# Kernel optimization log

Measured on AMD Instinct MI355X. Metric: run time of the kernel, lower is better.

Reference implementation:

```python
import jax, jax.numpy as jnp
import numpy as np

B, T, D, H, MLP_DIM = 4, 1024, 768, 12, 3072


def setup_inputs() -> dict:
    key = jax.random.key(0)
    ks = jax.random.split(key, 16)
    s = 0.02
    def n(i, shape):
        return jax.random.normal(ks[i], shape, jnp.float32) * s
    inp = {
        "x": jax.random.normal(ks[0], (B, T, D), jnp.float32),
        "y": jax.random.normal(ks[1], (B, T, D), jnp.float32),
        # self-attention (stream a = x, stream b = y), bias-free Linears
        "w_qkv_a": n(2, (D, 3 * D)), "w_out_a": n(3, (D, D)),
        "w_qkv_b": n(4, (D, 3 * D)), "w_out_b": n(5, (D, D)),
        # cross-attention
        "cw_qkv_a": n(6, (D, 3 * D)), "cw_out_a": n(7, (D, D)),
        "cw_qkv_b": n(8, (D, 3 * D)), "cw_out_b": n(9, (D, D)),
        # MLPs (Linear with bias)
        "mlp_a_w1": n(10, (D, MLP_DIM)), "mlp_a_b1": jnp.zeros((MLP_DIM,), jnp.float32),
        "mlp_a_w2": n(11, (MLP_DIM, D)), "mlp_a_b2": jnp.zeros((D,), jnp.float32),
        "mlp_b_w1": n(12, (D, MLP_DIM)), "mlp_b_b1": jnp.zeros((MLP_DIM,), jnp.float32),
        "mlp_b_w2": n(13, (MLP_DIM, D)), "mlp_b_b2": jnp.zeros((D,), jnp.float32),
    }
    for i in range(1, 7):
        inp[f"ln{i}_g"] = jnp.ones((D,), jnp.float32)
        inp[f"ln{i}_b"] = jnp.zeros((D,), jnp.float32)
    return inp


def _ln(x, g, b, eps=1e-5):
    m = x.mean(-1, keepdims=True)
    v = x.var(-1, keepdims=True)
    return (x - m) / jnp.sqrt(v + eps) * g + b


def _split_qkv(x, w, h):
    # faithful to einops 'b t (d k h) -> k b h t d' (d outermost, h innermost)
    qkv = x @ w                      # [b, t, 3D]
    b, t, _ = qkv.shape
    d = w.shape[0] // h
    qkv = qkv.reshape(b, t, d, 3, h).transpose(3, 0, 4, 1, 2)  # [3, b, h, t, d]
    return qkv[0], qkv[1], qkv[2]


def _attend(q, k, v, dk):
    a = jax.nn.softmax(jnp.einsum('bhid,bhjd->bhij', q, k) / dk, axis=-1)
    o = jnp.einsum('bhij,bhjd->bhid', a, v)
    b, h, t, d = o.shape
    return o.transpose(0, 2, 1, 3).reshape(b, t, h * d)


def reference(x, y,
              w_qkv_a, w_out_a, w_qkv_b, w_out_b,
              cw_qkv_a, cw_out_a, cw_qkv_b, cw_out_b,
              mlp_a_w1, mlp_a_b1, mlp_a_w2, mlp_a_b2,
              mlp_b_w1, mlp_b_b1, mlp_b_w2, mlp_b_b2,
              ln1_g, ln1_b, ln2_g, ln2_b, ln3_g, ln3_b,
              ln4_g, ln4_b, ln5_g, ln5_b, ln6_g, ln6_b):
    dk = np.float32(np.sqrt(D / H))
    # --- self-attention stage (pre-LN, residual); dropout = identity (eval) ---
    _x = _ln(x, ln1_g, ln1_b)
    _y = _ln(y, ln4_g, ln4_b)
    q, k, v = _split_qkv(_x, w_qkv_a, H)
    x = x + _attend(q, k, v, dk) @ w_out_a
    q, k, v = _split_qkv(_y, w_qkv_b, H)
    y = y + _attend(q, k, v, dk) @ w_out_b
    # --- cross-attention stage ---
    _x = _ln(x, ln2_g, ln2_b)
    _y = _ln(y, ln5_g, ln5_b)
    q1, k1, v1 = _split_qkv(_x, cw_qkv_a, H)
    q2, k2, v2 = _split_qkv(_y, cw_qkv_b, H)
    x = x + _attend(q2, k1, v1, dk) @ cw_out_a   # query from y, k/v from x
    y = y + _attend(q1, k2, v2, dk) @ cw_out_b   # query from x, k/v from y
    # --- MLP stage ---
    _x = _ln(x, ln3_g, ln3_b)
    _y = _ln(y, ln6_g, ln6_b)
    x = x + (jax.nn.gelu(_x @ mlp_a_w1 + mlp_a_b1, approximate=False) @ mlp_a_w2 + mlp_a_b2)
    y = y + (jax.nn.gelu(_y @ mlp_b_w1 + mlp_b_b1, approximate=False) @ mlp_b_w2 + mlp_b_b2)
    return (x, y)
```

## Files before the change

### kernel.cpp

```cpp
#include <hip/hip_runtime.h>
#include <hip/hip_bf16.h>

using bf16 = __hip_bfloat16;
typedef __bf16 bf16x8 __attribute__((ext_vector_type(8)));
typedef float f32x4 __attribute__((ext_vector_type(4)));

#define DEV __device__ __forceinline__

DEV void gload16(const void* g, void* l) {
  __builtin_amdgcn_global_load_lds((__attribute__((address_space(1))) void*)(g),
                                   (__attribute__((address_space(3))) void*)(l), 16, 0, 0);
}

DEV void mfma16(int4 a, int4 b, f32x4& c) {
  c = __builtin_amdgcn_mfma_f32_16x16x32_bf16(
      __builtin_bit_cast(bf16x8, a), __builtin_bit_cast(bf16x8, b), c, 0, 0, 0);
}

DEV unsigned short bfb(float x) { return __builtin_bit_cast(unsigned short, __float2bfloat16(x)); }

template<bool PERM>
__global__ __launch_bounds__(256) void wconv(const float* __restrict__ s0, const float* __restrict__ s1,
                                             const float* __restrict__ s2, const float* __restrict__ s3,
                                             bf16* d0, bf16* d1, bf16* d2, bf16* d3, int K, int N) {
  const float* S[4] = {s0, s1, s2, s3};
  bf16* Dd[4] = {d0, d1, d2, d3};
  const float* __restrict__ src = S[blockIdx.z];
  bf16* __restrict__ dst = Dd[blockIdx.z];
  __shared__ float tile[32][33];
  int tx = threadIdx.x, ty = threadIdx.y;
  int n0 = blockIdx.x * 32, k0 = blockIdx.y * 32;
#pragma unroll
  for (int i = 0; i < 4; i++) tile[ty + 8 * i][tx] = src[(size_t)(k0 + ty + 8 * i) * N + n0 + tx];
  __syncthreads();
#pragma unroll
  for (int i = 0; i < 4; i++) {
    int n = n0 + ty + 8 * i;
    int np;
    if (PERM) {
      int dd = n / 36; int r = n - dd * 36; int kk = r / 12; int h = r - kk * 12;
      np = kk * 768 + h * 64 + dd;
    } else np = n;
    dst[(size_t)np * K + k0 + tx] = __float2bfloat16(tile[tx][ty + 8 * i]);
  }
}

__global__ __launch_bounds__(192) void ln2(const float* __restrict__ xa, const float* __restrict__ xb,
                                           const float* __restrict__ ga, const float* __restrict__ ba,
                                           const float* __restrict__ gb, const float* __restrict__ bb,
                                           bf16* __restrict__ out) {
  int row = blockIdx.x;
  int s = row >> 12, r = row & 4095;
  const float* __restrict__ src = s ? xb : xa;
  const float* __restrict__ gp = s ? gb : ga;
  const float* __restrict__ bp = s ? bb : ba;
  int tid = threadIdx.x;
  float4 v = ((const float4*)(src + (size_t)r * 768))[tid];
  float sum = v.x + v.y + v.z + v.w;
  float sq = v.x * v.x + v.y * v.y + v.z * v.z + v.w * v.w;
#pragma unroll
  for (int o = 32; o; o >>= 1) { sum += __shfl_down(sum, o); sq += __shfl_down(sq, o); }
  __shared__ float red[6];
  int wv = tid >> 6;
  if ((tid & 63) == 0) { red[wv] = sum; red[wv + 3] = sq; }
  __syncthreads();
  sum = red[0] + red[1] + red[2];
  sq = red[3] + red[4] + red[5];
  float mean = sum * (1.f / 768.f);
  float var = sq * (1.f / 768.f) - mean * mean;
  float rstd = rsqrtf(var + 1e-5f);
  float4 g4 = ((const float4*)gp)[tid], b4 = ((const float4*)bp)[tid];
  ushort4 u;
  u.x = bfb((v.x - mean) * rstd * g4.x + b4.x);
  u.y = bfb((v.y - mean) * rstd * g4.y + b4.y);
  u.z = bfb((v.z - mean) * rstd * g4.z + b4.z);
  u.w = bfb((v.w - mean) * rstd * g4.w + b4.w);
  *(ushort4*)&out[(size_t)row * 768 + tid * 4] = u;
}

template<int EPI>
__global__ __launch_bounds__(256) void gemm_k(const bf16* __restrict__ A0, const bf16* __restrict__ A1,
                                              const bf16* __restrict__ Bt0, const bf16* __restrict__ Bt1,
                                              void* __restrict__ C0, void* __restrict__ C1,
                                              const float* __restrict__ bias0, const float* __restrict__ bias1,
                                              const float* __restrict__ res0, const float* __restrict__ res1,
                                              int N, int K) {
  int s = blockIdx.z;
  const bf16* __restrict__ A = s ? A1 : A0;
  const bf16* __restrict__ Bt = s ? Bt1 : Bt0;
  const float* __restrict__ bias = s ? bias1 : bias0;
  const float* __restrict__ res = s ? res1 : res0;
  int m0 = blockIdx.x * 128, n0 = blockIdx.y * 128;
  int tid = threadIdx.x, lane = tid & 63, w = tid >> 6;
  int g = lane >> 4, li = lane & 15;
  int wm = w >> 1, wn = w & 1;
  __shared__ __align__(16) bf16 As[2][128 * 32];
  __shared__ __align__(16) bf16 Bs[2][128 * 32];
  f32x4 acc[4][4];
  f32x4 zz = {0.f, 0.f, 0.f, 0.f};
#pragma unroll
  for (int i = 0; i < 4; i++)
#pragma unroll
    for (int j = 0; j < 4; j++) acc[i][j] = zz;

  const bf16* Ab = A + (size_t)m0 * K;
  const bf16* Bb = Bt + (size_t)n0 * K;
  int sw = (g ^ (li & 3)) << 3;

  auto stage = [&](int buf, int k0) {
#pragma unroll
    for (int i = 0; i < 2; i++) {
      int unit = w * 64 + i * 256 + lane;
      int row = unit >> 2, up = unit & 3;
      int col = (up ^ (row & 3)) << 3;
      gload16(Ab + (size_t)row * K + k0 + col, &As[buf][w * 512 + i * 2048]);
      gload16(Bb + (size_t)row * K + k0 + col, &Bs[buf][w * 512 + i * 2048]);
    }
  };

  const int nt = K >> 5;
  stage(0, 0);
  int cur = 0;
  for (int t = 0; t < nt; ++t) {
    __syncthreads();
    if (t + 1 < nt) stage(cur ^ 1, (t + 1) << 5);
    int4 af[4], bfr[4];
#pragma unroll
    for (int mi = 0; mi < 4; mi++) af[mi] = *(const int4*)&As[cur][(wm * 64 + mi * 16 + li) * 32 + sw];
#pragma unroll
    for (int ni = 0; ni < 4; ni++) bfr[ni] = *(const int4*)&Bs[cur][(wn * 64 + ni * 16 + li) * 32 + sw];
#pragma unroll
    for (int mi = 0; mi < 4; mi++)
#pragma unroll
      for (int ni = 0; ni < 4; ni++) mfma16(af[mi], bfr[ni], acc[mi][ni]);
    cur ^= 1;
  }

  int mrow0 = m0 + wm * 64;
  int col0 = n0 + wn * 64;
  if constexpr (EPI == 0) {
    bf16* qkv = (bf16*)C0;
#pragma unroll
    for (int mi = 0; mi < 4; mi++) {
      int mr = mrow0 + mi * 16 + 4 * g;
      int b = mr >> 10, t = mr & 1023;
#pragma unroll
      for (int ni = 0; ni < 4; ni++) {
        int col = col0 + ni * 16 + li;
        int kk = col / 768; int hd = col - kk * 768; int h = hd >> 6; int dd = hd & 63;
        size_t base = ((size_t)(kk * 2 + s) * 48 + b * 12 + h) * 65536;
        f32x4 v = acc[mi][ni];
        if (kk == 2) {
          ushort4 u; u.x = bfb(v[0]); u.y = bfb(v[1]); u.z = bfb(v[2]); u.w = bfb(v[3]);
          *(ushort4*)&qkv[base + (size_t)dd * 1024 + t] = u;
        } else {
#pragma unroll
          for (int ri = 0; ri < 4; ri++)
            qkv[base + (size_t)(t + ri) * 64 + dd] = __float2bfloat16(v[ri]);
        }
      }
    }
  } else if constexpr (EPI == 1) {
    float* C = (float*)(s ? C1 : C0);
#pragma unroll
    for (int mi = 0; mi < 4; mi++) {
      int mr = mrow0 + mi * 16 + 4 * g;
#pragma unroll
      for (int ni = 0; ni < 4; ni++) {
        int col = col0 + ni * 16 + li;
        float bv = bias ? bias[col] : 0.f;
#pragma unroll
        for (int ri = 0; ri < 4; ri++)
          C[(size_t)(mr + ri) * N + col] = res[(size_t)(mr + ri) * N + col] + acc[mi][ni][ri] + bv;
      }
    }
  } else {
    bf16* C = (bf16*)(s ? C1 : C0);
#pragma unroll
    for (int mi = 0; mi < 4; mi++) {
      int mr = mrow0 + mi * 16 + 4 * g;
#pragma unroll
      for (int ni = 0; ni < 4; ni++) {
        int col = col0 + ni * 16 + li;
        float bv = bias[col];
#pragma unroll
        for (int ri = 0; ri < 4; ri++) {
          float h = acc[mi][ni][ri] + bv;
          float o = 0.5f * h * (1.f + erff(h * 0.70710678118f));
          C[(size_t)(mr + ri) * N + col] = __float2bfloat16(o);
        }
      }
    }
  }
}

__global__ __launch_bounds__(256) void attn_k(const bf16* __restrict__ qkv, bf16* __restrict__ out, int cross) {
  int f = blockIdx.x;
  int qt = (f >> 3) & 7;
  int c = ((f >> 6) << 3) | (f & 7);
  int so = (c >= 48) ? 1 : 0;
  int bh = c - so * 48;
  int qs = cross ? 1 - so : so;
  const bf16* __restrict__ qp = qkv + ((size_t)qs * 48 + bh) * 65536;
  const bf16* __restrict__ kp = qkv + ((size_t)(2 + so) * 48 + bh) * 65536;
  const bf16* __restrict__ vp = qkv + ((size_t)(4 + so) * 48 + bh) * 65536;
  int tid = threadIdx.x, lane = tid & 63, w = tid >> 6, g = lane >> 4, li = lane & 15;
  __shared__ __align__(16) bf16 Ps[4][32 * 64];
  bf16* ps = Ps[w];
  int qr0 = qt * 128 + w * 32;
  int4 qf[2][2];
#pragma unroll
  for (int mi = 0; mi < 2; mi++)
#pragma unroll
    for (int ks = 0; ks < 2; ks++)
      qf[mi][ks] = *(const int4*)(qp + (size_t)(qr0 + mi * 16 + li) * 64 + ks * 32 + 8 * g);
  f32x4 o_acc[2][4];
  float m_run[2], l_run[2];
  f32x4 zz = {0.f, 0.f, 0.f, 0.f};
#pragma unroll
  for (int mi = 0; mi < 2; mi++) {
#pragma unroll
    for (int dj = 0; dj < 4; dj++) o_acc[mi][dj] = zz;
    m_run[mi] = -1e30f; l_run[mi] = 0.f;
  }
  const float C2 = 0.18033688011112042f;
  const int xsw = (li & 7);

#pragma unroll 2
  for (int kt = 0; kt < 16; ++kt) {
    f32x4 sacc[4][2];
#pragma unroll
    for (int nj = 0; nj < 4; nj++) { sacc[nj][0] = zz; sacc[nj][1] = zz; }
#pragma unroll
    for (int nj = 0; nj < 4; nj++) {
      const bf16* krow = kp + (size_t)(kt * 64 + nj * 16 + li) * 64 + 8 * g;
      int4 kf0 = *(const int4*)(krow);
      int4 kf1 = *(const int4*)(krow + 32);
      mfma16(kf0, qf[0][0], sacc[nj][0]); mfma16(kf1, qf[0][1], sacc[nj][0]);
      mfma16(kf0, qf[1][0], sacc[nj][1]); mfma16(kf1, qf[1][1], sacc[nj][1]);
    }
#pragma unroll
    for (int mi = 0; mi < 2; mi++) {
      float mx = sacc[0][mi][0];
#pragma unroll
      for (int nj = 0; nj < 4; nj++)
#pragma unroll
        for (int ri = 0; ri < 4; ri++) mx = fmaxf(mx, sacc[nj][mi][ri]);
      mx = fmaxf(mx, __shfl_xor(mx, 16));
      mx = fmaxf(mx, __shfl_xor(mx, 32));
      float mold = m_run[mi];
      float mnew = mold;
      if (!__all(mx <= mold)) {
        mnew = fmaxf(mold, mx);
        float alpha = exp2f((mold - mnew) * C2);
        l_run[mi] *= alpha;
#pragma unroll
        for (int dj = 0; dj < 4; dj++) o_acc[mi][dj] *= alpha;
        m_run[mi] = mnew;
      }
      float rs = 0.f;
#pragma unroll
      for (int nj = 0; nj < 4; nj++) {
        float p0 = exp2f((sacc[nj][mi][0] - mnew) * C2);
        float p1 = exp2f((sacc[nj][mi][1] - mnew) * C2);
        float p2 = exp2f((sacc[nj][mi][2] - mnew) * C2);
        float p3 = exp2f((sacc[nj][mi][3] - mnew) * C2);
        rs += (p0 + p1) + (p2 + p3);
        ushort4 u; u.x = bfb(p0); u.y = bfb(p1); u.z = bfb(p2); u.w = bfb(p3);
        *(ushort4*)&ps[(mi * 16 + li) * 64 + (((2 * nj + (g >> 1)) ^ xsw) << 3) + ((g & 1) << 2)] = u;
      }
      rs += __shfl_xor(rs, 16);
      rs += __shfl_xor(rs, 32);
      l_run[mi] += rs;
    }
#pragma unroll
    for (int ks2 = 0; ks2 < 2; ks2++) {
      int4 pa0 = *(const int4*)&ps[(0 * 16 + li) * 64 + (((4 * ks2 + g) ^ xsw) << 3)];
      int4 pa1 = *(const int4*)&ps[(1 * 16 + li) * 64 + (((4 * ks2 + g) ^ xsw) << 3)];
#pragma unroll
      for (int dj = 0; dj < 4; dj++) {
        int4 vf = *(const int4*)(vp + (size_t)(dj * 16 + li) * 1024 + kt * 64 + ks2 * 32 + 8 * g);
        mfma16(vf, pa0, o_acc[0][dj]);
        mfma16(vf, pa1, o_acc[1][dj]);
      }
    }
  }
  int b = bh / 12, h = bh - (bh / 12) * 12;
#pragma unroll
  for (int mi = 0; mi < 2; mi++) {
    float inv = 1.f / l_run[mi];
    int tq = qr0 + mi * 16 + li;
    size_t rowbase = ((size_t)so * 4096 + (size_t)b * 1024 + tq) * 768;
#pragma unroll
    for (int dj = 0; dj < 4; dj++) {
      ushort4 u;
      u.x = bfb(o_acc[mi][dj][0] * inv); u.y = bfb(o_acc[mi][dj][1] * inv);
      u.z = bfb(o_acc[mi][dj][2] * inv); u.w = bfb(o_acc[mi][dj][3] * inv);
      *(ushort4*)&out[rowbase + h * 64 + dj * 16 + 4 * g] = u;
    }
  }
}

extern "C" void kernel_launch(void* const* d_in, const int* in_sizes, int n_in,
                              void* d_out, int out_size, void* d_ws, size_t ws_size,
                              hipStream_t stream) {
  const float* x_in = (const float*)d_in[0];
  const float* y_in = (const float*)d_in[1];
  const float* w_qkv_a = (const float*)d_in[2];
  const float* w_out_a = (const float*)d_in[3];
  const float* w_qkv_b = (const float*)d_in[4];
  const float* w_out_b = (const float*)d_in[5];
  const float* cw_qkv_a = (const float*)d_in[6];
  const float* cw_out_a = (const float*)d_in[7];
  const float* cw_qkv_b = (const float*)d_in[8];
  const float* cw_out_b = (const float*)d_in[9];
  const float* w1a = (const float*)d_in[10]; const float* b1a = (const float*)d_in[11];
  const float* w2a = (const float*)d_in[12]; const float* b2a = (const float*)d_in[13];
  const float* w1b = (const float*)d_in[14]; const float* b1b = (const float*)d_in[15];
  const float* w2b = (const float*)d_in[16]; const float* b2b = (const float*)d_in[17];
  const float *lng[6], *lnb[6];
  for (int i = 0; i < 6; i++) { lng[i] = (const float*)d_in[18 + 2 * i]; lnb[i] = (const float*)d_in[19 + 2 * i]; }

  char* ws = (char*)d_ws;
  bf16* WQKV = (bf16*)ws;
  bf16* WOUT = (bf16*)(ws + 14155776);
  bf16* W1 = (bf16*)(ws + 18874368);
  bf16* W2 = (bf16*)(ws + 28311552);
  bf16* XN = (bf16*)(ws + 37748736);
  bf16* QKV = (bf16*)(ws + 50331648);
  bf16* AO = (bf16*)(ws + 88080384);
  bf16* MLPH = (bf16*)(ws + 50331648);
  float* X1 = (float*)(ws + 100663296);
  float* X2 = (float*)(ws + 125829120);
  float* OUT = (float*)d_out;

  dim3 tb(32, 8);
  wconv<true><<<dim3(72, 24, 4), tb, 0, stream>>>(w_qkv_a, w_qkv_b, cw_qkv_a, cw_qkv_b,
      WQKV, WQKV + 1769472, WQKV + 2 * 1769472, WQKV + 3 * 1769472, 768, 2304);
  wconv<false><<<dim3(24, 24, 4), tb, 0, stream>>>(w_out_a, w_out_b, cw_out_a, cw_out_b,
      WOUT, WOUT + 589824, WOUT + 2 * 589824, WOUT + 3 * 589824, 768, 768);
  wconv<false><<<dim3(96, 24, 2), tb, 0, stream>>>(w1a, w1b, nullptr, nullptr,
      W1, W1 + 2359296, nullptr, nullptr, 768, 3072);
  wconv<false><<<dim3(24, 96, 2), tb, 0, stream>>>(w2a, w2b, nullptr, nullptr,
      W2, W2 + 2359296, nullptr, nullptr, 3072, 768);

  ln2<<<8192, 192, 0, stream>>>(x_in, y_in, lng[0], lnb[0], lng[3], lnb[3], XN);
  gemm_k<0><<<dim3(32, 18, 2), 256, 0, stream>>>(XN, XN + 3145728, WQKV, WQKV + 1769472,
      QKV, nullptr, nullptr, nullptr, nullptr, nullptr, 2304, 768);
  attn_k<<<dim3(768, 1, 1), 256, 0, stream>>>(QKV, AO, 0);
  gemm_k<1><<<dim3(32, 6, 2), 256, 0, stream>>>(AO, AO + 3145728, WOUT, WOUT + 589824,
      X1, X1 + 3145728, nullptr, nullptr, x_in, y_in, 768, 768);
  ln2<<<8192, 192, 0, stream>>>(X1, X1 + 3145728, lng[1], lnb[1], lng[4], lnb[4], XN);
  gemm_k<0><<<dim3(32, 18, 2), 256, 0, stream>>>(XN, XN + 3145728, WQKV + 2 * 1769472, WQKV + 3 * 1769472,
      QKV, nullptr, nullptr, nullptr, nullptr, nullptr, 2304, 768);
  attn_k<<<dim3(768, 1, 1), 256, 0, stream>>>(QKV, AO, 1);
  gemm_k<1><<<dim3(32, 6, 2), 256, 0, stream>>>(AO, AO + 3145728, WOUT + 2 * 589824, WOUT + 3 * 589824,
      X2, X2 + 3145728, nullptr, nullptr, X1, X1 + 3145728, 768, 768);
  ln2<<<8192, 192, 0, stream>>>(X2, X2 + 3145728, lng[2], lnb[2], lng[5], lnb[5], XN);
  gemm_k<2><<<dim3(32, 24, 2), 256, 0, stream>>>(XN, XN + 3145728, W1, W1 + 2359296,
      MLPH, MLPH + 12582912, b1a, b1b, nullptr, nullptr, 3072, 768);
  gemm_k<1><<<dim3(32, 6, 2), 256, 0, stream>>>(MLPH, MLPH + 12582912, W2, W2 + 2359296,
      OUT, OUT + 3145728, b2a, b2b, X2, X2 + 3145728, 768, 3072);
}
```

Before: 519.3 us.

## Use single-wave attention blocks with early K/V prefetch and deferred row-sum reduction

The attention kernel now runs one 64-thread wave per block (3072 blocks, launch bounds allowing several waves per SIMD) instead of four waves per 256-thread block. All K and V fragments for a key tile are loaded into registers at the start of each iteration so their latency overlaps the QK^T and softmax math. The per-tile cross-lane reduction of the row sum is moved to the end of the kernel, and the P tile in shared memory gets a padded row stride of 80. Holding more fragments in registers raises register pressure and may reduce occupancy, and removing the unroll pragma changes the instruction schedule.

Result: slower. 640.4 us (+23.3%).

```diff
diff --git a/kernel.cpp b/kernel.cpp
--- a/kernel.cpp
+++ b/kernel.cpp
@@ -194,20 +194,19 @@
   }
 }
 
-__global__ __launch_bounds__(256) void attn_k(const bf16* __restrict__ qkv, bf16* __restrict__ out, int cross) {
-  int f = blockIdx.x;
-  int qt = (f >> 3) & 7;
-  int c = ((f >> 6) << 3) | (f & 7);
+__global__ __launch_bounds__(64, 4) void attn_k(const bf16* __restrict__ qkv, bf16* __restrict__ out, int cross) {
+  int b0 = blockIdx.x;
+  int gl = b0 & 7, rr = b0 >> 3, qb = rr & 31, gh = rr >> 5;
+  int c = gh * 8 + gl;
   int so = (c >= 48) ? 1 : 0;
   int bh = c - so * 48;
   int qs = cross ? 1 - so : so;
   const bf16* __restrict__ qp = qkv + ((size_t)qs * 48 + bh) * 65536;
   const bf16* __restrict__ kp = qkv + ((size_t)(2 + so) * 48 + bh) * 65536;
   const bf16* __restrict__ vp = qkv + ((size_t)(4 + so) * 48 + bh) * 65536;
-  int tid = threadIdx.x, lane = tid & 63, w = tid >> 6, g = lane >> 4, li = lane & 15;
-  __shared__ __align__(16) bf16 Ps[4][32 * 64];
-  bf16* ps = Ps[w];
-  int qr0 = qt * 128 + w * 32;
+  int lane = threadIdx.x & 63, g = lane >> 4, li = lane & 15;
+  __shared__ __align__(16) bf16 ps[32 * 80];
+  int qr0 = qb * 32;
   int4 qf[2][2];
 #pragma unroll
   for (int mi = 0; mi < 2; mi++)
@@ -226,26 +225,35 @@
   const float C2 = 0.18033688011112042f;
   const int xsw = (li & 7);
 
-#pragma unroll 2
   for (int kt = 0; kt < 16; ++kt) {
-    f32x4 sacc[4][2];
-#pragma unroll
-    for (int nj = 0; nj < 4; nj++) { sacc[nj][0] = zz; sacc[nj][1] = zz; }
+    int4 kf[4][2];
 #pragma unroll
     for (int nj = 0; nj < 4; nj++) {
       const bf16* krow = kp + (size_t)(kt * 64 + nj * 16 + li) * 64 + 8 * g;
-      int4 kf0 = *(const int4*)(krow);
-      int4 kf1 = *(const int4*)(krow + 32);
-      mfma16(kf0, qf[0][0], sacc[nj][0]); mfma16(kf1, qf[0][1], sacc[nj][0]);
-      mfma16(kf0, qf[1][0], sacc[nj][1]); mfma16(kf1, qf[1][1], sacc[nj][1]);
-    }
+      kf[nj][0] = *(const int4*)(krow);
+      kf[nj][1] = *(const int4*)(krow + 32);
+    }
+    int4 vf[2][4];
+#pragma unroll
+    for (int ks2 = 0; ks2 < 2; ks2++)
+#pragma unroll
+      for (int dj = 0; dj < 4; dj++)
+        vf[ks2][dj] = *(const int4*)(vp + (size_t)(dj * 16 + li) * 1024 + kt * 64 + ks2 * 32 + 8 * g);
 #pragma unroll
     for (int mi = 0; mi < 2; mi++) {
-      float mx = sacc[0][mi][0];
-#pragma unroll
-      for (int nj = 0; nj < 4; nj++)
-#pragma unroll
-        for (int ri = 0; ri < 4; ri++) mx = fmaxf(mx, sacc[nj][mi][ri]);
+      f32x4 sc[4];
+      sc[0] = zz; sc[1] = zz; sc[2] = zz; sc[3] = zz;
+#pragma unroll
+      for (int nj = 0; nj < 4; nj++) {
+        mfma16(kf[nj][0], qf[mi][0], sc[nj]);
+        mfma16(kf[nj][1], qf[mi][1], sc[nj]);
+      }
+      float a0 = fmaxf(fmaxf(sc[0][0], sc[0][1]), sc[0][2]);
+      float a1 = fmaxf(fmaxf(sc[0][3], sc[1][0]), sc[1][1]);
+      float a2 = fmaxf(fmaxf(sc[1][2], sc[1][3]), sc[2][0]);
+      float a3 = fmaxf(fmaxf(sc[2][1], sc[2][2]), sc[2][3]);
+      float a4 = fmaxf(fmaxf(sc[3][0], sc[3][1]), sc[3][2]);
+      float mx = fmaxf(fmaxf(fmaxf(a0, a1), fmaxf(a2, a3)), fmaxf(a4, sc[3][3]));
       mx = fmaxf(mx, __shfl_xor(mx, 16));
       mx = fmaxf(mx, __shfl_xor(mx, 32));
       float mold = m_run[mi];
@@ -261,34 +269,34 @@
       float rs = 0.f;
 #pragma unroll
       for (int nj = 0; nj < 4; nj++) {
-        float p0 = exp2f((sacc[nj][mi][0] - mnew) * C2);
-        float p1 = exp2f((sacc[nj][mi][1] - mnew) * C2);
-        float p2 = exp2f((sacc[nj][mi][2] - mnew) * C2);
-        float p3 = exp2f((sacc[nj][mi][3] - mnew) * C2);
+        float p0 = exp2f((sc[nj][0] - mnew) * C2);
+        float p1 = exp2f((sc[nj][1] - mnew) * C2);
+        float p2 = exp2f((sc[nj][2] - mnew) * C2);
+        float p3 = exp2f((sc[nj][3] - mnew) * C2);
         rs += (p0 + p1) + (p2 + p3);
         ushort4 u; u.x = bfb(p0); u.y = bfb(p1); u.z = bfb(p2); u.w = bfb(p3);
-        *(ushort4*)&ps[(mi * 16 + li) * 64 + (((2 * nj + (g >> 1)) ^ xsw) << 3) + ((g & 1) << 2)] = u;
-      }
-      rs += __shfl_xor(rs, 16);
-      rs += __shfl_xor(rs, 32);
+        *(ushort4*)&ps[(mi * 16 + li) * 80 + (((2 * nj + (g >> 1)) ^ xsw) << 3) + ((g & 1) << 2)] = u;
+      }
       l_run[mi] += rs;
     }
 #pragma unroll
     for (int ks2 = 0; ks2 < 2; ks2++) {
-      int4 pa0 = *(const int4*)&ps[(0 * 16 + li) * 64 + (((4 * ks2 + g) ^ xsw) << 3)];
-      int4 pa1 = *(const int4*)&ps[(1 * 16 + li) * 64 + (((4 * ks2 + g) ^ xsw) << 3)];
+      int4 pa0 = *(const int4*)&ps[(0 * 16 + li) * 80 + (((4 * ks2 + g) ^ xsw) << 3)];
+      int4 pa1 = *(const int4*)&ps[(1 * 16 + li) * 80 + (((4 * ks2 + g) ^ xsw) << 3)];
 #pragma unroll
       for (int dj = 0; dj < 4; dj++) {
-        int4 vf = *(const int4*)(vp + (size_t)(dj * 16 + li) * 1024 + kt * 64 + ks2 * 32 + 8 * g);
-        mfma16(vf, pa0, o_acc[0][dj]);
-        mfma16(vf, pa1, o_acc[1][dj]);
+        mfma16(vf[ks2][dj], pa0, o_acc[0][dj]);
+        mfma16(vf[ks2][dj], pa1, o_acc[1][dj]);
       }
     }
   }
   int b = bh / 12, h = bh - (bh / 12) * 12;
 #pragma unroll
   for (int mi = 0; mi < 2; mi++) {
-    float inv = 1.f / l_run[mi];
+    float lt = l_run[mi];
+    lt += __shfl_xor(lt, 16);
+    lt += __shfl_xor(lt, 32);
+    float inv = 1.f / lt;
     int tq = qr0 + mi * 16 + li;
     size_t rowbase = ((size_t)so * 4096 + (size_t)b * 1024 + tq) * 768;
 #pragma unroll
@@ -347,13 +355,13 @@
   ln2<<<8192, 192, 0, stream>>>(x_in, y_in, lng[0], lnb[0], lng[3], lnb[3], XN);
   gemm_k<0><<<dim3(32, 18, 2), 256, 0, stream>>>(XN, XN + 3145728, WQKV, WQKV + 1769472,
       QKV, nullptr, nullptr, nullptr, nullptr, nullptr, 2304, 768);
-  attn_k<<<dim3(768, 1, 1), 256, 0, stream>>>(QKV, AO, 0);
+  attn_k<<<dim3(3072, 1, 1), 64, 0, stream>>>(QKV, AO, 0);
   gemm_k<1><<<dim3(32, 6, 2), 256, 0, stream>>>(AO, AO + 3145728, WOUT, WOUT + 589824,
       X1, X1 + 3145728, nullptr, nullptr, x_in, y_in, 768, 768);
   ln2<<<8192, 192, 0, stream>>>(X1, X1 + 3145728, lng[1], lnb[1], lng[4], lnb[4], XN);
   gemm_k<0><<<dim3(32, 18, 2), 256, 0, stream>>>(XN, XN + 3145728, WQKV + 2 * 1769472, WQKV + 3 * 1769472,
       QKV, nullptr, nullptr, nullptr, nullptr, nullptr, 2304, 768);
-  attn_k<<<dim3(768, 1, 1), 256, 0, stream>>>(QKV, AO, 1);
+  attn_k<<<dim3(3072, 1, 1), 64, 0, stream>>>(QKV, AO, 1);
   gemm_k<1><<<dim3(32, 6, 2), 256, 0, stream>>>(AO, AO + 3145728, WOUT + 2 * 589824, WOUT + 3 * 589824,
       X2, X2 + 3145728, nullptr, nullptr, X1, X1 + 3145728, 768, 768);
   ln2<<<8192, 192, 0, stream>>>(X2, X2 + 3145728, lng[2], lnb[2], lng[5], lnb[5], XN);
```

## Software-pipeline K/V loads in attention and use a fast polynomial GELU

Applied to the files above, without the earlier changes.

Restructures the attention inner loop to prefetch the next K tile into registers and issue V loads early so they overlap with softmax, raises MFMA wave priority around the matrix blocks, and sets an occupancy hint of 3 blocks per CU. It pads the P tile rows in shared memory to 72 elements, and defers the row-sum cross-lane reduction to the end of the loop. It also replaces erff in the MLP GELU epilogue with an Abramowitz-Stegun polynomial erf using rcp and fast exp. This trades extra register pressure and slightly lower GELU accuracy for less memory stall and cheaper transcendental work.

After: 533.9 us. 2.8% more time.

```diff
diff --git a/kernel.cpp b/kernel.cpp
--- a/kernel.cpp
+++ b/kernel.cpp
@@ -18,6 +18,17 @@
 }
 
 DEV unsigned short bfb(float x) { return __builtin_bit_cast(unsigned short, __float2bfloat16(x)); }
+
+DEV float gelu_f(float h) {
+  float xr = h * 0.70710678118f;
+  float ax = fabsf(xr);
+  float t = __builtin_amdgcn_rcpf(fmaf(0.3275911f, ax, 1.f));
+  float poly = fmaf(fmaf(fmaf(fmaf(1.061405429f, t, -1.453152027f), t, 1.421413741f),
+                         t, -0.284496736f), t, 0.254829592f) * t;
+  float e = __expf(-xr * xr);
+  float erfv = copysignf(1.f - poly * e, xr);
+  return 0.5f * h * (1.f + erfv);
+}
 
 template<bool PERM>
 __global__ __launch_bounds__(256) void wconv(const float* __restrict__ s0, const float* __restrict__ s1,
@@ -184,17 +195,14 @@
         int col = col0 + ni * 16 + li;
         float bv = bias[col];
 #pragma unroll
-        for (int ri = 0; ri < 4; ri++) {
-          float h = acc[mi][ni][ri] + bv;
-          float o = 0.5f * h * (1.f + erff(h * 0.70710678118f));
-          C[(size_t)(mr + ri) * N + col] = __float2bfloat16(o);
-        }
+        for (int ri = 0; ri < 4; ri++)
+          C[(size_t)(mr + ri) * N + col] = __float2bfloat16(gelu_f(acc[mi][ni][ri] + bv));
       }
     }
   }
 }
 
-__global__ __launch_bounds__(256) void attn_k(const bf16* __restrict__ qkv, bf16* __restrict__ out, int cross) {
+__global__ __launch_bounds__(256, 3) void attn_k(const bf16* __restrict__ qkv, bf16* __restrict__ out, int cross) {
   int f = blockIdx.x;
   int qt = (f >> 3) & 7;
   int c = ((f >> 6) << 3) | (f & 7);
@@ -205,7 +213,7 @@
   const bf16* __restrict__ kp = qkv + ((size_t)(2 + so) * 48 + bh) * 65536;
   const bf16* __restrict__ vp = qkv + ((size_t)(4 + so) * 48 + bh) * 65536;
   int tid = threadIdx.x, lane = tid & 63, w = tid >> 6, g = lane >> 4, li = lane & 15;
-  __shared__ __align__(16) bf16 Ps[4][32 * 64];
+  __shared__ __align__(16) bf16 Ps[4][32 * 72];
   bf16* ps = Ps[w];
   int qr0 = qt * 128 + w * 32;
   int4 qf[2][2];
@@ -224,71 +232,98 @@
     m_run[mi] = -1e30f; l_run[mi] = 0.f;
   }
   const float C2 = 0.18033688011112042f;
-  const int xsw = (li & 7);
-
-#pragma unroll 2
+  const int xsw = li & 7;
+  const bf16* krow = kp + (size_t)li * 64 + 8 * g;
+  const bf16* vrow = vp + (size_t)li * 1024 + 8 * g;
+
+  int4 kf[4][2];
+#pragma unroll
+  for (int nj = 0; nj < 4; nj++) {
+    kf[nj][0] = *(const int4*)(krow + nj * 1024);
+    kf[nj][1] = *(const int4*)(krow + nj * 1024 + 32);
+  }
+
+  auto do_softmax = [&](int mi, f32x4 (&sc)[4][2]) {
+    float mx = sc[0][mi][0];
+#pragma unroll
+    for (int nj = 0; nj < 4; nj++)
+#pragma unroll
+      for (int ri = 0; ri < 4; ri++) mx = fmaxf(mx, sc[nj][mi][ri]);
+    mx = fmaxf(mx, __shfl_xor(mx, 16));
+    mx = fmaxf(mx, __shfl_xor(mx, 32));
+    float mold = m_run[mi];
+    float mnew = mold;
+    if (!__all(mx <= mold)) {
+      mnew = fmaxf(mold, mx);
+      float alpha = exp2f((mold - mnew) * C2);
+      l_run[mi] *= alpha;
+#pragma unroll
+      for (int dj = 0; dj < 4; dj++) o_acc[mi][dj] *= alpha;
+      m_run[mi] = mnew;
+    }
+    float rs = 0.f;
+#pragma unroll
+    for (int nj = 0; nj < 4; nj++) {
+      float p0 = exp2f((sc[nj][mi][0] - mnew) * C2);
+      float p1 = exp2f((sc[nj][mi][1] - mnew) * C2);
+      float p2 = exp2f((sc[nj][mi][2] - mnew) * C2);
+      float p3 = exp2f((sc[nj][mi][3] - mnew) * C2);
+      rs += (p0 + p1) + (p2 + p3);
+      ushort4 u; u.x = bfb(p0); u.y = bfb(p1); u.z = bfb(p2); u.w = bfb(p3);
+      *(ushort4*)&ps[(mi * 16 + li) * 72 + (((2 * nj + (g >> 1)) ^ xsw) << 3) + ((g & 1) << 2)] = u;
+    }
+    l_run[mi] += rs;
+  };
+
+#pragma unroll 1
   for (int kt = 0; kt < 16; ++kt) {
     f32x4 sacc[4][2];
 #pragma unroll
     for (int nj = 0; nj < 4; nj++) { sacc[nj][0] = zz; sacc[nj][1] = zz; }
+    __builtin_amdgcn_s_setprio(1);
 #pragma unroll
     for (int nj = 0; nj < 4; nj++) {
-      const bf16* krow = kp + (size_t)(kt * 64 + nj * 16 + li) * 64 + 8 * g;
-      int4 kf0 = *(const int4*)(krow);
-      int4 kf1 = *(const int4*)(krow + 32);
-      mfma16(kf0, qf[0][0], sacc[nj][0]); mfma16(kf1, qf[0][1], sacc[nj][0]);
-      mfma16(kf0, qf[1][0], sacc[nj][1]); mfma16(kf1, qf[1][1], sacc[nj][1]);
-    }
-#pragma unroll
-    for (int mi = 0; mi < 2; mi++) {
-      float mx = sacc[0][mi][0];
-#pragma unroll
-      for (int nj = 0; nj < 4; nj++)
-#pragma unroll
-        for (int ri = 0; ri < 4; ri++) mx = fmaxf(mx, sacc[nj][mi][ri]);
-      mx = fmaxf(mx, __shfl_xor(mx, 16));
-      mx = fmaxf(mx, __shfl_xor(mx, 32));
-      float mold = m_run[mi];
-      float mnew = mold;
-      if (!__all(mx <= mold)) {
-        mnew = fmaxf(mold, mx);
-        float alpha = exp2f((mold - mnew) * C2);
-        l_run[mi] *= alpha;
-#pragma unroll
-        for (int dj = 0; dj < 4; dj++) o_acc[mi][dj] *= alpha;
-        m_run[mi] = mnew;
+      mfma16(kf[nj][0], qf[0][0], sacc[nj][0]); mfma16(kf[nj][1], qf[0][1], sacc[nj][0]);
+      mfma16(kf[nj][0], qf[1][0], sacc[nj][1]); mfma16(kf[nj][1], qf[1][1], sacc[nj][1]);
+    }
+    __builtin_amdgcn_s_setprio(0);
+    int4 vf0[4];
+#pragma unroll
+    for (int dj = 0; dj < 4; dj++) vf0[dj] = *(const int4*)(vrow + dj * 16384 + kt * 64);
+    if (kt < 15) {
+      const bf16* kb = krow + (kt + 1) * 4096;
+#pragma unroll
+      for (int nj = 0; nj < 4; nj++) {
+        kf[nj][0] = *(const int4*)(kb + nj * 1024);
+        kf[nj][1] = *(const int4*)(kb + nj * 1024 + 32);
       }
-      float rs = 0.f;
-#pragma unroll
-      for (int nj = 0; nj < 4; nj++) {
-        float p0 = exp2f((sacc[nj][mi][0] - mnew) * C2);
-        float p1 = exp2f((sacc[nj][mi][1] - mnew) * C2);
-        float p2 = exp2f((sacc[nj][mi][2] - mnew) * C2);
-        float p3 = exp2f((sacc[nj][mi][3] - mnew) * C2);
-        rs += (p0 + p1) + (p2 + p3);
-        ushort4 u; u.x = bfb(p0); u.y = bfb(p1); u.z = bfb(p2); u.w = bfb(p3);
-        *(ushort4*)&ps[(mi * 16 + li) * 64 + (((2 * nj + (g >> 1)) ^ xsw) << 3) + ((g & 1) << 2)] = u;
-      }
-      rs += __shfl_xor(rs, 16);
-      rs += __shfl_xor(rs, 32);
-      l_run[mi] += rs;
-    }
-#pragma unroll
-    for (int ks2 = 0; ks2 < 2; ks2++) {
-      int4 pa0 = *(const int4*)&ps[(0 * 16 + li) * 64 + (((4 * ks2 + g) ^ xsw) << 3)];
-      int4 pa1 = *(const int4*)&ps[(1 * 16 + li) * 64 + (((4 * ks2 + g) ^ xsw) << 3)];
-#pragma unroll
-      for (int dj = 0; dj < 4; dj++) {
-        int4 vf = *(const int4*)(vp + (size_t)(dj * 16 + li) * 1024 + kt * 64 + ks2 * 32 + 8 * g);
-        mfma16(vf, pa0, o_acc[0][dj]);
-        mfma16(vf, pa1, o_acc[1][dj]);
-      }
-    }
+    }
+    do_softmax(0, sacc);
+    int4 vf1[4];
+#pragma unroll
+    for (int dj = 0; dj < 4; dj++) vf1[dj] = *(const int4*)(vrow + dj * 16384 + kt * 64 + 32);
+    do_softmax(1, sacc);
+    int4 pa00 = *(const int4*)&ps[li * 72 + ((g ^ xsw) << 3)];
+    int4 pa01 = *(const int4*)&ps[(16 + li) * 72 + ((g ^ xsw) << 3)];
+    int4 pa10 = *(const int4*)&ps[li * 72 + (((4 + g) ^ xsw) << 3)];
+    int4 pa11 = *(const int4*)&ps[(16 + li) * 72 + (((4 + g) ^ xsw) << 3)];
+    __builtin_amdgcn_s_setprio(1);
+#pragma unroll
+    for (int dj = 0; dj < 4; dj++) {
+      mfma16(vf0[dj], pa00, o_acc[0][dj]);
+      mfma16(vf0[dj], pa01, o_acc[1][dj]);
+      mfma16(vf1[dj], pa10, o_acc[0][dj]);
+      mfma16(vf1[dj], pa11, o_acc[1][dj]);
+    }
+    __builtin_amdgcn_s_setprio(0);
   }
   int b = bh / 12, h = bh - (bh / 12) * 12;
 #pragma unroll
   for (int mi = 0; mi < 2; mi++) {
-    float inv = 1.f / l_run[mi];
+    float lt = l_run[mi];
+    lt += __shfl_xor(lt, 16);
+    lt += __shfl_xor(lt, 32);
+    float inv = 1.f / lt;
     int tq = qr0 + mi * 16 + li;
     size_t rowbase = ((size_t)so * 4096 + (size_t)b * 1024 + tq) * 768;
 #pragma unroll
```

## Split attention over two KV chunks with combine kernel; use fast GELU

Applied to the files above, without the earlier changes.

The attention kernel now splits the 1024-key range into two halves and launches twice as many blocks. Each block writes unnormalized partial outputs plus its running max and row sum to workspace, and a new combine kernel merges the two halves with log-sum-exp weights. The goal is higher occupancy and parallelism on the GPU, at the cost of an extra kernel launch and about 25 MB of extra partial-output traffic per attention call. The MLP GELU epilogue replaces erff with an Abramowitz-Stegun polynomial using a fast reciprocal and exp, and the probability packing switches to the v_cvt_pk_bf16_f32 instruction. The row-sum cross-lane shuffle now runs once at the end instead of every tile.

New measurement: 562.3 us. 1.08x slower.

```diff
diff --git a/kernel.cpp b/kernel.cpp
--- a/kernel.cpp
+++ b/kernel.cpp
@@ -18,6 +18,23 @@
 }
 
 DEV unsigned short bfb(float x) { return __builtin_bit_cast(unsigned short, __float2bfloat16(x)); }
+
+DEV int cvtpk(float lo, float hi) {
+  int r;
+  asm("v_cvt_pk_bf16_f32 %0, %1, %2" : "=v"(r) : "v"(lo), "v"(hi));
+  return r;
+}
+
+DEV float gelu_f(float h) {
+  float xr = h * 0.70710678118f;
+  float ax = fabsf(xr);
+  float t = __builtin_amdgcn_rcpf(fmaf(0.3275911f, ax, 1.f));
+  float poly = fmaf(fmaf(fmaf(fmaf(1.061405429f, t, -1.453152027f), t, 1.421413741f),
+                         t, -0.284496736f), t, 0.254829592f) * t;
+  float e = __expf(-xr * xr);
+  float erfv = copysignf(1.f - poly * e, xr);
+  return 0.5f * h * (1.f + erfv);
+}
 
 template<bool PERM>
 __global__ __launch_bounds__(256) void wconv(const float* __restrict__ s0, const float* __restrict__ s1,
@@ -184,20 +201,19 @@
         int col = col0 + ni * 16 + li;
         float bv = bias[col];
 #pragma unroll
-        for (int ri = 0; ri < 4; ri++) {
-          float h = acc[mi][ni][ri] + bv;
-          float o = 0.5f * h * (1.f + erff(h * 0.70710678118f));
-          C[(size_t)(mr + ri) * N + col] = __float2bfloat16(o);
-        }
-      }
-    }
-  }
-}
-
-__global__ __launch_bounds__(256) void attn_k(const bf16* __restrict__ qkv, bf16* __restrict__ out, int cross) {
-  int f = blockIdx.x;
-  int qt = (f >> 3) & 7;
-  int c = ((f >> 6) << 3) | (f & 7);
+        for (int ri = 0; ri < 4; ri++)
+          C[(size_t)(mr + ri) * N + col] = __float2bfloat16(gelu_f(acc[mi][ni][ri] + bv));
+      }
+    }
+  }
+}
+
+__global__ __launch_bounds__(256) void attn_k(const bf16* __restrict__ qkv, bf16* __restrict__ OP,
+                                              float* __restrict__ ML, int cross) {
+  int b0 = blockIdx.x;
+  int gl = b0 & 7, rr = b0 >> 3;
+  int qt = rr & 7, ck = (rr >> 3) & 1, gh = rr >> 4;
+  int c = gh * 8 + gl;
   int so = (c >= 48) ? 1 : 0;
   int bh = c - so * 48;
   int qs = cross ? 1 - so : so;
@@ -225,9 +241,10 @@
   }
   const float C2 = 0.18033688011112042f;
   const int xsw = (li & 7);
+  const int kt_end = ck * 8 + 8;
 
 #pragma unroll 2
-  for (int kt = 0; kt < 16; ++kt) {
+  for (int kt = ck * 8; kt < kt_end; ++kt) {
     f32x4 sacc[4][2];
 #pragma unroll
     for (int nj = 0; nj < 4; nj++) { sacc[nj][0] = zz; sacc[nj][1] = zz; }
@@ -266,11 +283,9 @@
         float p2 = exp2f((sacc[nj][mi][2] - mnew) * C2);
         float p3 = exp2f((sacc[nj][mi][3] - mnew) * C2);
         rs += (p0 + p1) + (p2 + p3);
-        ushort4 u; u.x = bfb(p0); u.y = bfb(p1); u.z = bfb(p2); u.w = bfb(p3);
-        *(ushort4*)&ps[(mi * 16 + li) * 64 + (((2 * nj + (g >> 1)) ^ xsw) << 3) + ((g & 1) << 2)] = u;
-      }
-      rs += __shfl_xor(rs, 16);
-      rs += __shfl_xor(rs, 32);
+        int2 u2; u2.x = cvtpk(p0, p1); u2.y = cvtpk(p2, p3);
+        *(int2*)&ps[(mi * 16 + li) * 64 + (((2 * nj + (g >> 1)) ^ xsw) << 3) + ((g & 1) << 2)] = u2;
+      }
       l_run[mi] += rs;
     }
 #pragma unroll
@@ -285,20 +300,48 @@
       }
     }
   }
-  int b = bh / 12, h = bh - (bh / 12) * 12;
+  size_t pb = ((size_t)(ck * 2 + so) * 48 + bh) * 65536;
+  float* mlp = ML + ((size_t)(ck * 2 + so) * 48 + bh) * 2048;
 #pragma unroll
   for (int mi = 0; mi < 2; mi++) {
-    float inv = 1.f / l_run[mi];
-    int tq = qr0 + mi * 16 + li;
-    size_t rowbase = ((size_t)so * 4096 + (size_t)b * 1024 + tq) * 768;
+    float lt = l_run[mi];
+    lt += __shfl_xor(lt, 16);
+    lt += __shfl_xor(lt, 32);
+    int q = qr0 + mi * 16 + li;
+    if (g == 0) { mlp[q] = m_run[mi]; mlp[1024 + q] = lt; }
 #pragma unroll
     for (int dj = 0; dj < 4; dj++) {
       ushort4 u;
-      u.x = bfb(o_acc[mi][dj][0] * inv); u.y = bfb(o_acc[mi][dj][1] * inv);
-      u.z = bfb(o_acc[mi][dj][2] * inv); u.w = bfb(o_acc[mi][dj][3] * inv);
-      *(ushort4*)&out[rowbase + h * 64 + dj * 16 + 4 * g] = u;
-    }
-  }
+      u.x = bfb(o_acc[mi][dj][0]); u.y = bfb(o_acc[mi][dj][1]);
+      u.z = bfb(o_acc[mi][dj][2]); u.w = bfb(o_acc[mi][dj][3]);
+      *(ushort4*)&OP[pb + (size_t)q * 64 + dj * 16 + 4 * g] = u;
+    }
+  }
+}
+
+__global__ __launch_bounds__(256) void attn_combine(const bf16* __restrict__ OP,
+                                                    const float* __restrict__ ML,
+                                                    bf16* __restrict__ out) {
+  int r = blockIdx.x * 4 + (threadIdx.x >> 6);
+  int lane = threadIdx.x & 63;
+  int so = (r >= 49152) ? 1 : 0;
+  int rr = r - so * 49152;
+  int bh = rr >> 10, q = rr & 1023;
+  size_t i0 = (size_t)so * 48 + bh;
+  size_t i1 = (size_t)(2 + so) * 48 + bh;
+  const float* ml0 = ML + i0 * 2048;
+  const float* ml1 = ML + i1 * 2048;
+  float m0 = ml0[q], l0 = ml0[1024 + q];
+  float m1 = ml1[q], l1 = ml1[1024 + q];
+  float m = fmaxf(m0, m1);
+  const float C2 = 0.18033688011112042f;
+  float w0 = exp2f((m0 - m) * C2), w1 = exp2f((m1 - m) * C2);
+  float rl = 1.f / (w0 * l0 + w1 * l1);
+  float o0 = __bfloat162float(OP[i0 * 65536 + (size_t)q * 64 + lane]);
+  float o1 = __bfloat162float(OP[i1 * 65536 + (size_t)q * 64 + lane]);
+  int b = bh / 12, h = bh - (bh / 12) * 12;
+  out[((size_t)so * 4096 + (size_t)b * 1024 + q) * 768 + h * 64 + lane] =
+      __float2bfloat16((w0 * o0 + w1 * o1) * rl);
 }
 
 extern "C" void kernel_launch(void* const* d_in, const int* in_sizes, int n_in,
@@ -332,6 +375,8 @@
   bf16* MLPH = (bf16*)(ws + 50331648);
   float* X1 = (float*)(ws + 100663296);
   float* X2 = (float*)(ws + 125829120);
+  bf16* OPp = (bf16*)(ws + 125829120);
+  float* MLp = (float*)(ws + 37748736 + 8388608);
   float* OUT = (float*)d_out;
 
   dim3 tb(32, 8);
@@ -347,13 +392,15 @@
   ln2<<<8192, 192, 0, stream>>>(x_in, y_in, lng[0], lnb[0], lng[3], lnb[3], XN);
   gemm_k<0><<<dim3(32, 18, 2), 256, 0, stream>>>(XN, XN + 3145728, WQKV, WQKV + 1769472,
       QKV, nullptr, nullptr, nullptr, nullptr, nullptr, 2304, 768);
-  attn_k<<<dim3(768, 1, 1), 256, 0, stream>>>(QKV, AO, 0);
+  attn_k<<<dim3(1536, 1, 1), 256, 0, stream>>>(QKV, OPp, MLp, 0);
+  attn_combine<<<dim3(24576, 1, 1), 256, 0, stream>>>(OPp, MLp, AO);
   gemm_k<1><<<dim3(32, 6, 2), 256, 0, stream>>>(AO, AO + 3145728, WOUT, WOUT + 589824,
       X1, X1 + 3145728, nullptr, nullptr, x_in, y_in, 768, 768);
   ln2<<<8192, 192, 0, stream>>>(X1, X1 + 3145728, lng[1], lnb[1], lng[4], lnb[4], XN);
   gemm_k<0><<<dim3(32, 18, 2), 256, 0, stream>>>(XN, XN + 3145728, WQKV + 2 * 1769472, WQKV + 3 * 1769472,
       QKV, nullptr, nullptr, nullptr, nullptr, nullptr, 2304, 768);
-  attn_k<<<dim3(768, 1, 1), 256, 0, stream>>>(QKV, AO, 1);
+  attn_k<<<dim3(1536, 1, 1), 256, 0, stream>>>(QKV, OPp, MLp, 1);
+  attn_combine<<<dim3(24576, 1, 1), 256, 0, stream>>>(OPp, MLp, AO);
   gemm_k<1><<<dim3(32, 6, 2), 256, 0, stream>>>(AO, AO + 3145728, WOUT + 2 * 589824, WOUT + 3 * 589824,
       X2, X2 + 3145728, nullptr, nullptr, X1, X1 + 3145728, 768, 768);
   ln2<<<8192, 192, 0, stream>>>(X2, X2 + 3145728, lng[2], lnb[2], lng[5], lnb[5], XN);
```
